# Performance work log

Measured on AMD Instinct MI355X. Metric: run time of the kernel, lower is better.

## Reference

```python
import jax, jax.numpy as jnp
import numpy as np

ROT_DIM = 32  # rotary sub-dimension hardcoded in the original module


def apply_rope(x, rope):
    # x: [B, T, H, hd], rope: [T, ROT_DIM//2, 2]
    T = x.shape[1]
    rc = rope[:T][:, None]            # [T, 1, 16, 2]
    cos, sin = rc[..., 0], rc[..., 1]  # [T, 1, 16]
    x_rot, x_pass = x[..., :ROT_DIM], x[..., ROT_DIM:]
    x1, x2 = x_rot[..., :ROT_DIM // 2], x_rot[..., ROT_DIM // 2:]
    return jnp.concatenate([x1 * cos - x2 * sin, x2 * cos + x1 * sin, x_pass], axis=-1)


def setup_inputs() -> dict:
    key = jax.random.key(0)
    ks = jax.random.split(key, 6)
    B, T, C, H = 4, 1024, 2048, 32
    hd = C // H
    x = jax.random.normal(ks[0], (B, T, C), dtype=jnp.float32)
    mask = jnp.tril(jnp.ones((T, T), dtype=bool))  # causal, True = attend
    index = jnp.arange(T, dtype=jnp.int64) if jax.config.jax_enable_x64 else jnp.arange(T, dtype=jnp.int32)
    # realistic rotary cos/sin cache
    inv_freq = 1.0 / (10000.0 ** (np.arange(0, ROT_DIM, 2, dtype=np.float32) / ROT_DIM))
    ang = np.arange(T, dtype=np.float32)[:, None] * inv_freq[None, :]  # [T, 16]
    rope = jnp.asarray(np.stack([np.cos(ang), np.sin(ang)], axis=-1))   # [T, 16, 2]
    s = 1.0 / np.sqrt(C)
    Wqkv_w = jax.random.normal(ks[1], (3 * C, C), dtype=jnp.float32) * s
    Wqkv_b = jax.random.normal(ks[2], (3 * C,), dtype=jnp.float32) * 0.01
    out_w = jax.random.normal(ks[3], (C, C), dtype=jnp.float32) * s
    out_b = jax.random.normal(ks[4], (C,), dtype=jnp.float32) * 0.01
    k_cache = jnp.zeros((B, H, T, hd), dtype=jnp.float32)
    v_cache = jnp.zeros((B, H, T, hd), dtype=jnp.float32)
    return {"x": x, "mask": mask, "index": index, "rope": rope,
            "Wqkv_w": Wqkv_w, "Wqkv_b": Wqkv_b, "out_w": out_w, "out_b": out_b,
            "k_cache": k_cache, "v_cache": v_cache}


def reference(x, mask, index, rope, Wqkv_w, Wqkv_b, out_w, out_b, k_cache, v_cache):
    B, T, C = x.shape
    H = 32
    hd = C // H
    qkv = x @ Wqkv_w.T + Wqkv_b                 # [B, T, 3C]
    q, k, v = jnp.split(qkv, 3, axis=-1)
    q = q.reshape(B, T, H, hd)
    k = k.reshape(B, T, H, hd)
    v = v.reshape(B, T, H, hd)
    q = apply_rope(q, rope)
    k = apply_rope(k, rope)
    q = q.transpose(0, 2, 1, 3)                 # [B, H, T, hd]
    k = k.transpose(0, 2, 1, 3)
    v = v.transpose(0, 2, 1, 3)
    # KV-cache scatter update; index = arange(T) covers the full cache, so the
    # subsequent slice [:, :, :index[-1]+1] is the whole cache (static shape).
    k_full = k_cache.at[:, :, index].set(k)
    v_full = v_cache.at[:, :, index].set(v)
    scores = jnp.einsum('bhqd,bhkd->bhqk', q, k_full) / jnp.sqrt(jnp.asarray(hd, x.dtype))
    scores = jnp.where(mask, scores, jnp.finfo(x.dtype).min)
    attn = jax.nn.softmax(scores, axis=-1)
    ctx = jnp.einsum('bhqk,bhkd->bhqd', attn, v_full)
    ctx = ctx.transpose(0, 2, 1, 3).reshape(B, T, C)
    return ctx @ out_w.T + out_b
```

## Files before the change

### kernel.cpp

```cpp
#include <hip/hip_runtime.h>

typedef unsigned short u16;
typedef unsigned int u32;
typedef __bf16 bf16x8 __attribute__((ext_vector_type(8)));
typedef float floatx4 __attribute__((ext_vector_type(4)));
typedef u16 u16x4 __attribute__((ext_vector_type(4)));
typedef u16 u16x8 __attribute__((ext_vector_type(8)));
typedef u32 u32x2 __attribute__((ext_vector_type(2)));

#define B_ 4
#define T_ 1024
#define C_ 2048
#define H_ 32
#define HD_ 64

__device__ __forceinline__ float b2f(u16 u) {
    u32 x = ((u32)u) << 16;
    return __builtin_bit_cast(float, x);
}
__device__ __forceinline__ u16 f2b(float f) {
    u32 i = __builtin_bit_cast(u32, f);
    u32 r = (i + 0x7FFFu + ((i >> 16) & 1u)) >> 16;
    return (u16)r;
}
__device__ __forceinline__ u32 pack2(float a, float b) {
    const u32 ua = __builtin_bit_cast(u32, a) + 0x8000u;
    const u32 ub = __builtin_bit_cast(u32, b) + 0x8000u;
    return __builtin_amdgcn_perm(ub, ua, 0x07060302u);
}

#define GLOAD16(gp, lp) __builtin_amdgcn_global_load_lds( \
    (const __attribute__((address_space(1))) void*)(gp),  \
    (__attribute__((address_space(3))) void*)(lp), 16, 0, 0)

__global__ __launch_bounds__(256) void convert_bf16(const float* __restrict__ src,
                                                    u16* __restrict__ dst, int n4) {
    const int stride = gridDim.x * 256;
    for (int i = blockIdx.x * 256 + threadIdx.x; i < n4; i += stride) {
        const floatx4 v = *(const floatx4*)(src + (size_t)i * 4);
        const u32x2 h = {pack2(v.x, v.y), pack2(v.z, v.w)};
        *(u32x2*)(dst + (size_t)i * 4) = h;
    }
}

template <int MODE>
__global__ __launch_bounds__(256) void gemm_bt(const u16* __restrict__ A,
                                               const u16* __restrict__ W,
                                               const float* __restrict__ bias,
                                               const float* __restrict__ rope,
                                               void* __restrict__ o0v,
                                               u16* __restrict__ o1,
                                               u16* __restrict__ o2) {
    const int Kdim = 2048;
    __shared__ __align__(16) u16 As[128 * 64];
    __shared__ __align__(16) u16 Bs[128 * 64];

    const int tid = threadIdx.x;
    const int w = tid >> 6, lane = tid & 63;
    const int wr = w >> 1, wc = w & 1;
    const int quad = lane >> 4, l15 = lane & 15;
    const int mBase = blockIdx.y * 128, nBase = blockIdx.x * 128;

    floatx4 acc[4][4] = {};

    const int lrow = lane >> 3;
    const int lcol = ((lane & 7) ^ lrow) * 8;
    const u16* Ap = A + (size_t)(mBase + lrow) * Kdim + lcol;
    const u16* Wp = W + (size_t)(nBase + lrow) * Kdim + lcol;

    const int xk = l15 & 7;

    for (int k0 = 0; k0 < Kdim; k0 += 64) {
#pragma unroll
        for (int i = 0; i < 4; i++) {
            const int c = i * 4 + w;
            GLOAD16(Ap + (size_t)c * 8 * Kdim + k0, &As[c * 512]);
            GLOAD16(Wp + (size_t)c * 8 * Kdim + k0, &Bs[c * 512]);
        }
        __syncthreads();
#pragma unroll
        for (int ks = 0; ks < 64; ks += 32) {
            bf16x8 af[4], bfr[4];
#pragma unroll
            for (int i = 0; i < 4; i++) {
                const int co = (((ks >> 3) + quad) ^ xk) * 8;
                af[i] = *(const bf16x8*)&As[(wr * 64 + i * 16 + l15) * 64 + co];
            }
#pragma unroll
            for (int j = 0; j < 4; j++) {
                const int co = (((ks >> 3) + quad) ^ xk) * 8;
                bfr[j] = *(const bf16x8*)&Bs[(wc * 64 + j * 16 + l15) * 64 + co];
            }
#pragma unroll
            for (int i = 0; i < 4; i++)
#pragma unroll
                for (int j = 0; j < 4; j++)
                    acc[i][j] = __builtin_amdgcn_mfma_f32_16x16x32_bf16(af[i], bfr[j], acc[i][j], 0, 0, 0);
        }
        __syncthreads();
    }

    const int nq = nBase + wc * 64;
    float bv[4];
#pragma unroll
    for (int j = 0; j < 4; j++) bv[j] = bias[nq + j * 16 + l15];

    if (MODE == 0) {
        const int region = nq >> 11;
        const int h = (nq & 2047) >> 6;
        const int d = l15;
        u16* dst = (region == 0) ? (u16*)o0v : ((region == 1) ? o1 : o2);
#pragma unroll
        for (int i = 0; i < 4; i++) {
#pragma unroll
            for (int r = 0; r < 4; r++) {
                const int m = mBase + wr * 64 + i * 16 + quad * 4 + r;
                const int b = m >> 10, t = m & 1023;
                float v0 = acc[i][0][r] + bv[0];
                float v1 = acc[i][1][r] + bv[1];
                float v2 = acc[i][2][r] + bv[2];
                float v3 = acc[i][3][r] + bv[3];
                const size_t base = ((size_t)(b * H_ + h) * T_ + t) * HD_;
                if (region < 2) {
                    const float cz = rope[t * 32 + d * 2];
                    const float sz = rope[t * 32 + d * 2 + 1];
                    const float n0 = v0 * cz - v1 * sz;
                    const float n1 = v1 * cz + v0 * sz;
                    dst[base + d] = f2b(n0);
                    dst[base + 16 + d] = f2b(n1);
                } else {
                    dst[base + d] = f2b(v0);
                    dst[base + 16 + d] = f2b(v1);
                }
                dst[base + 32 + d] = f2b(v2);
                dst[base + 48 + d] = f2b(v3);
            }
        }
    } else {
        float* outf = (float*)o0v;
#pragma unroll
        for (int i = 0; i < 4; i++)
#pragma unroll
            for (int r = 0; r < 4; r++) {
                const int m = mBase + wr * 64 + i * 16 + quad * 4 + r;
                const size_t o = (size_t)m * 2048 + nq;
#pragma unroll
                for (int j = 0; j < 4; j++)
                    outf[o + j * 16 + l15] = acc[i][j][r] + bv[j];
            }
    }
}

#define VT_STR 72

__global__ __launch_bounds__(256) void attn_mfma(const u16* __restrict__ qT,
                                                 const u16* __restrict__ kT,
                                                 const u16* __restrict__ vT,
                                                 u16* __restrict__ ctx) {
    __shared__ __align__(16) u16 Vt[64 * VT_STR];
    __shared__ __align__(16) u16 Pt[4 * 16 * VT_STR];

    const int tid = threadIdx.x;
    const int w = tid >> 6, lane = tid & 63;
    const int quad = lane >> 4, l15 = lane & 15;
    const int qt = 15 - (int)blockIdx.x;
    const int bh = blockIdx.y;
    const size_t headBase = (size_t)bh * (T_ * HD_);

    bf16x8 qf[2];
    {
        const u16* qrow = qT + headBase + ((size_t)qt * 64 + w * 16 + l15) * HD_ + quad * 8;
        qf[0] = __builtin_bit_cast(bf16x8, *(const u16x8*)(qrow));
        qf[1] = __builtin_bit_cast(bf16x8, *(const u16x8*)(qrow + 32));
    }

    u16* myPt = &Pt[w * 16 * VT_STR];
    const int vhd = tid & 63, vkb = tid >> 6;
    float m_i = -1e30f, l_i = 0.f;
    floatx4 oacc[4] = {};

    for (int kt = 0; kt <= qt; kt++) {
        const u16* kp = kT + headBase + (size_t)kt * 64 * HD_;
        const u16* vp = vT + headBase + (size_t)kt * 64 * HD_;

        u16 vreg[16];
#pragma unroll
        for (int c = 0; c < 16; c++)
            vreg[c] = vp[(vkb * 16 + c) * HD_ + vhd];

        floatx4 st[4] = {};
#pragma unroll
        for (int mi = 0; mi < 4; mi++) {
            const u16* krow = kp + (mi * 16 + l15) * HD_ + quad * 8;
            const bf16x8 kf0 = __builtin_bit_cast(bf16x8, *(const u16x8*)(krow));
            const bf16x8 kf1 = __builtin_bit_cast(bf16x8, *(const u16x8*)(krow + 32));
            st[mi] = __builtin_amdgcn_mfma_f32_16x16x32_bf16(kf0, qf[0], st[mi], 0, 0, 0);
            st[mi] = __builtin_amdgcn_mfma_f32_16x16x32_bf16(kf1, qf[1], st[mi], 0, 0, 0);
        }

        __syncthreads();
#pragma unroll
        for (int c4 = 0; c4 < 4; c4++) {
            const u16x4 vv = {vreg[c4 * 4], vreg[c4 * 4 + 1], vreg[c4 * 4 + 2], vreg[c4 * 4 + 3]};
            *(u16x4*)&Vt[vhd * VT_STR + vkb * 16 + c4 * 4] = vv;
        }
        __syncthreads();

        float pmax = -1e30f;
#pragma unroll
        for (int mi = 0; mi < 4; mi++)
#pragma unroll
            for (int r = 0; r < 4; r++) {
                float sv = st[mi][r] * 0.125f;
                if (kt == qt && (mi * 16 + quad * 4 + r) > (w * 16 + l15)) sv = -1e30f;
                st[mi][r] = sv;
                pmax = fmaxf(pmax, sv);
            }
        pmax = fmaxf(pmax, __shfl_xor(pmax, 16, 64));
        pmax = fmaxf(pmax, __shfl_xor(pmax, 32, 64));
        const float mnew = fmaxf(m_i, pmax);
        const float alpha = __expf(m_i - mnew);
        m_i = mnew;

        float psum = 0.f;
#pragma unroll
        for (int mi = 0; mi < 4; mi++) {
            u16x4 pk;
#pragma unroll
            for (int r = 0; r < 4; r++) {
                const float p = __expf(st[mi][r] - mnew);
                psum += p;
                pk[r] = f2b(p);
            }
            *(u16x4*)&myPt[l15 * VT_STR + mi * 16 + quad * 4] = pk;
        }
        psum += __shfl_xor(psum, 16, 64);
        psum += __shfl_xor(psum, 32, 64);
        l_i = l_i * alpha + psum;

#pragma unroll
        for (int mi = 0; mi < 4; mi++) oacc[mi] *= alpha;

        bf16x8 pf[2];
        pf[0] = __builtin_bit_cast(bf16x8, *(const u16x8*)&myPt[l15 * VT_STR + quad * 8]);
        pf[1] = __builtin_bit_cast(bf16x8, *(const u16x8*)&myPt[l15 * VT_STR + 32 + quad * 8]);
#pragma unroll
        for (int mi = 0; mi < 4; mi++) {
            const bf16x8 vf0 = __builtin_bit_cast(bf16x8, *(const u16x8*)&Vt[(mi * 16 + l15) * VT_STR + quad * 8]);
            const bf16x8 vf1 = __builtin_bit_cast(bf16x8, *(const u16x8*)&Vt[(mi * 16 + l15) * VT_STR + 32 + quad * 8]);
            oacc[mi] = __builtin_amdgcn_mfma_f32_16x16x32_bf16(vf0, pf[0], oacc[mi], 0, 0, 0);
            oacc[mi] = __builtin_amdgcn_mfma_f32_16x16x32_bf16(vf1, pf[1], oacc[mi], 0, 0, 0);
        }
    }

    const float inv = 1.0f / l_i;
    const int b = bh >> 5, h = bh & 31;
    const int t = qt * 64 + w * 16 + l15;
    u16* cp = ctx + ((size_t)(b * T_ + t)) * C_ + h * HD_;
#pragma unroll
    for (int mi = 0; mi < 4; mi++) {
        const u16x4 ov = {f2b(oacc[mi][0] * inv), f2b(oacc[mi][1] * inv),
                          f2b(oacc[mi][2] * inv), f2b(oacc[mi][3] * inv)};
        *(u16x4*)(cp + mi * 16 + quad * 4) = ov;
    }
}

extern "C" void kernel_launch(void* const* d_in, const int* in_sizes, int n_in,
                              void* d_out, int out_size, void* d_ws, size_t ws_size,
                              hipStream_t stream) {
    const float* x      = (const float*)d_in[0];
    const float* rope   = (const float*)d_in[3];
    const float* Wqkv_w = (const float*)d_in[4];
    const float* Wqkv_b = (const float*)d_in[5];
    const float* out_w  = (const float*)d_in[6];
    const float* out_b  = (const float*)d_in[7];
    float* out = (float*)d_out;

    const size_t headElems = (size_t)B_ * H_ * T_ * HD_;
    u16* xb    = (u16*)d_ws;
    u16* wqkvb = xb + headElems;
    u16* outwb = wqkvb + 12582912;
    u16* qTp   = outwb + 4194304;
    u16* kTp   = qTp + headElems;
    u16* vTp   = kTp + headElems;
    u16* ctx   = xb;

    convert_bf16<<<dim3(2048), 256, 0, stream>>>(x, xb, 2097152);
    convert_bf16<<<dim3(3072), 256, 0, stream>>>(Wqkv_w, wqkvb, 3145728);
    convert_bf16<<<dim3(1024), 256, 0, stream>>>(out_w, outwb, 1048576);

    gemm_bt<0><<<dim3(48, 32), 256, 0, stream>>>(xb, wqkvb, Wqkv_b, rope, qTp, kTp, vTp);
    attn_mfma<<<dim3(16, 128), 256, 0, stream>>>(qTp, kTp, vTp, ctx);
    gemm_bt<1><<<dim3(16, 32), 256, 0, stream>>>(ctx, outwb, out_b, rope, out, nullptr, nullptr);
}
```

Baseline: 477.3 us.

## Pre-transpose V into a separate buffer and drop the LDS V staging in attention

Adds a transpose_v kernel that writes V as [bh, hd, T] into the now-unused Wqkv bf16 workspace. The attention kernel then loads V fragments straight from global memory as 16-byte vectors, with no per-tile scalar gather, LDS write and two __syncthreads. This removes the per-tile block barriers and uncoalesced 2-byte V loads. In exchange it adds an extra kernel launch and a full pass over V, and reuses the wqkvb buffer after the QKV GEMM is done with it.

Result: slower. 571.3 us (+19.7%).

```diff
diff --git a/kernel.cpp b/kernel.cpp
--- a/kernel.cpp
+++ b/kernel.cpp
@@ -41,6 +41,27 @@
         const u32x2 h = {pack2(v.x, v.y), pack2(v.z, v.w)};
         *(u32x2*)(dst + (size_t)i * 4) = h;
     }
+}
+
+__global__ __launch_bounds__(256) void transpose_v(const u16* __restrict__ vin,
+                                                   u16* __restrict__ vout) {
+    __shared__ u16 L[64][72];
+    const int tid = threadIdx.x;
+    const int bh = blockIdx.y, t0 = blockIdx.x * 64;
+    const u16* src = vin + (size_t)bh * (T_ * HD_) + (size_t)t0 * HD_;
+    const int r = tid >> 2, c = (tid & 3) * 16;
+    *(u16x8*)&L[r][c]     = *(const u16x8*)(src + r * HD_ + c);
+    *(u16x8*)&L[r][c + 8] = *(const u16x8*)(src + r * HD_ + c + 8);
+    __syncthreads();
+    const int d = tid >> 2, ts = (tid & 3) * 16;
+    u16x8 o0, o1;
+#pragma unroll
+    for (int t = 0; t < 8; t++) o0[t] = L[ts + t][d];
+#pragma unroll
+    for (int t = 0; t < 8; t++) o1[t] = L[ts + 8 + t][d];
+    u16* dst = vout + (size_t)bh * (T_ * HD_) + (size_t)d * T_ + t0 + ts;
+    *(u16x8*)dst = o0;
+    *(u16x8*)(dst + 8) = o1;
 }
 
 template <int MODE>
@@ -155,9 +176,8 @@
 
 __global__ __launch_bounds__(256) void attn_mfma(const u16* __restrict__ qT,
                                                  const u16* __restrict__ kT,
-                                                 const u16* __restrict__ vT,
+                                                 const u16* __restrict__ vTt,
                                                  u16* __restrict__ ctx) {
-    __shared__ __align__(16) u16 Vt[64 * VT_STR];
     __shared__ __align__(16) u16 Pt[4 * 16 * VT_STR];
 
     const int tid = threadIdx.x;
@@ -175,18 +195,13 @@
     }
 
     u16* myPt = &Pt[w * 16 * VT_STR];
-    const int vhd = tid & 63, vkb = tid >> 6;
     float m_i = -1e30f, l_i = 0.f;
     floatx4 oacc[4] = {};
 
+    const u16* vtBase = vTt + headBase + (size_t)l15 * T_ + (size_t)quad * 8;
+
     for (int kt = 0; kt <= qt; kt++) {
         const u16* kp = kT + headBase + (size_t)kt * 64 * HD_;
-        const u16* vp = vT + headBase + (size_t)kt * 64 * HD_;
-
-        u16 vreg[16];
-#pragma unroll
-        for (int c = 0; c < 16; c++)
-            vreg[c] = vp[(vkb * 16 + c) * HD_ + vhd];
 
         floatx4 st[4] = {};
 #pragma unroll
@@ -198,14 +213,6 @@
             st[mi] = __builtin_amdgcn_mfma_f32_16x16x32_bf16(kf1, qf[1], st[mi], 0, 0, 0);
         }
 
-        __syncthreads();
-#pragma unroll
-        for (int c4 = 0; c4 < 4; c4++) {
-            const u16x4 vv = {vreg[c4 * 4], vreg[c4 * 4 + 1], vreg[c4 * 4 + 2], vreg[c4 * 4 + 3]};
-            *(u16x4*)&Vt[vhd * VT_STR + vkb * 16 + c4 * 4] = vv;
-        }
-        __syncthreads();
-
         float pmax = -1e30f;
 #pragma unroll
         for (int mi = 0; mi < 4; mi++)
@@ -244,10 +251,12 @@
         bf16x8 pf[2];
         pf[0] = __builtin_bit_cast(bf16x8, *(const u16x8*)&myPt[l15 * VT_STR + quad * 8]);
         pf[1] = __builtin_bit_cast(bf16x8, *(const u16x8*)&myPt[l15 * VT_STR + 32 + quad * 8]);
+        const u16* vk = vtBase + kt * 64;
 #pragma unroll
         for (int mi = 0; mi < 4; mi++) {
-            const bf16x8 vf0 = __builtin_bit_cast(bf16x8, *(const u16x8*)&Vt[(mi * 16 + l15) * VT_STR + quad * 8]);
-            const bf16x8 vf1 = __builtin_bit_cast(bf16x8, *(const u16x8*)&Vt[(mi * 16 + l15) * VT_STR + 32 + quad * 8]);
+            const u16* vrow = vk + (size_t)mi * 16 * T_;
+            const bf16x8 vf0 = __builtin_bit_cast(bf16x8, *(const u16x8*)(vrow));
+            const bf16x8 vf1 = __builtin_bit_cast(bf16x8, *(const u16x8*)(vrow + 32));
             oacc[mi] = __builtin_amdgcn_mfma_f32_16x16x32_bf16(vf0, pf[0], oacc[mi], 0, 0, 0);
             oacc[mi] = __builtin_amdgcn_mfma_f32_16x16x32_bf16(vf1, pf[1], oacc[mi], 0, 0, 0);
         }
@@ -284,12 +293,14 @@
     u16* kTp   = qTp + headElems;
     u16* vTp   = kTp + headElems;
     u16* ctx   = xb;
+    u16* vTt   = wqkvb;
 
     convert_bf16<<<dim3(2048), 256, 0, stream>>>(x, xb, 2097152);
     convert_bf16<<<dim3(3072), 256, 0, stream>>>(Wqkv_w, wqkvb, 3145728);
     convert_bf16<<<dim3(1024), 256, 0, stream>>>(out_w, outwb, 1048576);
 
     gemm_bt<0><<<dim3(48, 32), 256, 0, stream>>>(xb, wqkvb, Wqkv_b, rope, qTp, kTp, vTp);
-    attn_mfma<<<dim3(16, 128), 256, 0, stream>>>(qTp, kTp, vTp, ctx);
+    transpose_v<<<dim3(16, 128), 256, 0, stream>>>(vTp, vTt);
+    attn_mfma<<<dim3(16, 128), 256, 0, stream>>>(qTp, kTp, vTt, ctx);
     gemm_bt<1><<<dim3(16, 32), 256, 0, stream>>>(ctx, outwb, out_b, rope, out, nullptr, nullptr);
 }
```
